# Performance work log

Hardware: AMD Instinct MI355X
Metric: run time of the kernel (lower is better)

The kernel has to match this reference:

```python
import jax, jax.numpy as jnp
import numpy as np

N, E = 100_000, 1_600_000
NFEAT, NHID, HEADS = 128, 128, 2
FOUT = NHID // 2  # per-head out feats (DGL GATConv(nfeat, nhid//2, num_heads=2))
NEG_SLOPE = 0.2
LN_EPS = 1e-5


def setup_inputs() -> dict:
    key = jax.random.key(0)
    ks = jax.random.split(key, 10)
    h = jax.random.normal(ks[0], (N, NFEAT), dtype=jnp.float32)
    src = jax.random.randint(ks[1], (E,), 0, N, dtype=jnp.int32)
    dst = jax.random.randint(ks[2], (E,), 0, N, dtype=jnp.int32)
    # GATConv params
    W = jax.random.normal(ks[3], (NFEAT, HEADS * FOUT), dtype=jnp.float32) / np.sqrt(NFEAT)
    attn_l = jax.random.normal(ks[4], (HEADS, FOUT), dtype=jnp.float32) * 0.1
    attn_r = jax.random.normal(ks[5], (HEADS, FOUT), dtype=jnp.float32) * 0.1
    bias = jnp.zeros((HEADS * FOUT,), dtype=jnp.float32)
    # LayerNorm params
    gamma = jnp.ones((NHID,), dtype=jnp.float32)
    beta = jnp.zeros((NHID,), dtype=jnp.float32)
    return {"h": h, "src": src, "dst": dst, "W": W, "attn_l": attn_l,
            "attn_r": attn_r, "bias": bias, "gamma": gamma, "beta": beta}


def reference(h, src, dst, W, attn_l, attn_r, bias, gamma, beta):
    # --- GATConv ---
    feat = (h @ W).reshape(N, HEADS, FOUT)                 # [N,H,F]
    el = jnp.einsum('nhf,hf->nh', feat, attn_l)            # [N,H]
    er = jnp.einsum('nhf,hf->nh', feat, attn_r)            # [N,H]
    e = jax.nn.leaky_relu(el[src] + er[dst], NEG_SLOPE)    # [E,H]
    # edge softmax over incoming edges of each dst node
    emax = jax.ops.segment_max(e, dst, num_segments=N)     # [N,H] (-inf for empty ok)
    expe = jnp.exp(e - emax[dst])                          # [E,H]
    denom = jax.ops.segment_sum(expe, dst, num_segments=N) # [N,H]
    alpha = expe / denom[dst]                              # [E,H]
    msg = feat[src] * alpha[:, :, None]                    # [E,H,F]
    out = jax.ops.segment_sum(msg, dst, num_segments=N)    # [N,H,F]
    x = out.reshape(N, HEADS * FOUT) + bias                # [N,NHID]
    # --- LayerNorm ---
    mu = jnp.mean(x, axis=-1, keepdims=True)
    var = jnp.mean(jnp.square(x - mu), axis=-1, keepdims=True)
    return gamma * (x - mu) * jax.lax.rsqrt(var + LN_EPS) + beta
```

## Files before the change

### kernel.cpp

```cpp
#include <hip/hip_runtime.h>
#include <hip/hip_bf16.h>

#define NFEAT 128
#define NHID  128
#define HEADS 2
#define FOUT  64
#define NEG_SLOPE 0.2f
#define LN_EPS 1e-5f
#define NPART 8
#define ECHUNK 1024
#define PACK_BLOCKS 64
#define STRIDE 64

typedef __attribute__((ext_vector_type(8))) short  short8;
typedef __attribute__((ext_vector_type(4))) float  floatx4;
typedef unsigned short ushort_t;

__device__ __forceinline__ unsigned short f32_to_bf16_bits(float x) {
    unsigned int u = __float_as_uint(x);
    unsigned int r = (u + 0x7FFF + ((u >> 16) & 1)) >> 16;
    return (unsigned short)r;
}

__global__ __launch_bounds__(256) void histscatter_pack_kernel(
    const float* __restrict__ W, ushort_t* __restrict__ pBhi,
    ushort_t* __restrict__ pBlo, const int* __restrict__ src,
    const int* __restrict__ dst, int* __restrict__ deg,
    int* __restrict__ csr_src, int E, int N)
{
    if (blockIdx.x < PACK_BLOCKS) {
        int i = blockIdx.x * 256 + threadIdx.x;
        int k = i >> 7, n = i & 127;
        float x = W[i];
        unsigned short hb = f32_to_bf16_bits(x);
        float hf = __uint_as_float(((unsigned int)hb) << 16);
        unsigned short lb = f32_to_bf16_bits(x - hf);
        int t = n >> 4, s = k >> 5, q = (k >> 3) & 3, j = k & 7;
        int lanei = (q << 4) | (n & 15);
        int idx = ((t * 4 + s) * 64 + lanei) * 8 + j;
        pBhi[idx] = hb; pBlo[idx] = lb;
        return;
    }
    int bid   = blockIdx.x - PACK_BLOCKS;
    int p     = bid & (NPART - 1);
    int chunk = bid >> 3;
    int base  = chunk * ECHUNK + threadIdx.x * 4;
    int lo = (int)(((long long)p       * N) / NPART);
    int hi = (int)(((long long)(p + 1) * N) / NPART);
    if (base + 3 < E) {
        int4 d4 = *(const int4*)(dst + base);
        int dd[4] = {d4.x, d4.y, d4.z, d4.w};
#pragma unroll
        for (int k = 0; k < 4; k++) {
            int d = dd[k];
            if (d >= lo && d < hi) {
                int pos = atomicAdd(&deg[d], 1);
                if (pos < STRIDE)
                    csr_src[(size_t)d * STRIDE + pos] = src[base + k];
            }
        }
    } else {
        for (int k = 0; k < 4; k++) {
            int i = base + k;
            if (i < E) {
                int d = dst[i];
                if (d >= lo && d < hi) {
                    int pos = atomicAdd(&deg[d], 1);
                    if (pos < STRIDE)
                        csr_src[(size_t)d * STRIDE + pos] = src[i];
                }
            }
        }
    }
}

__global__ __launch_bounds__(256) void gemm_mfma_kernel(
    const float* __restrict__ h,
    const ushort_t* __restrict__ pBhi, const ushort_t* __restrict__ pBlo,
    const float* __restrict__ attn_l, const float* __restrict__ attn_r,
    ushort_t* __restrict__ featb, float* __restrict__ el,
    float* __restrict__ er, int N)
{
    const int lane = threadIdx.x & 63;
    const int wv   = threadIdx.x >> 6;
    const int r0   = blockIdx.x * 64 + wv * 16;
    const int m    = lane & 15;
    const int q    = lane >> 4;
    int row  = r0 + m;
    int rowc = min(row, N - 1);
    const float* hrow = h + (size_t)rowc * NFEAT + q * 8;

    floatx4 acc[8];
#pragma unroll
    for (int t = 0; t < 8; t++) acc[t] = (floatx4){0.f, 0.f, 0.f, 0.f};

#pragma unroll
    for (int s = 0; s < 4; ++s) {
        float4 a0 = *(const float4*)(hrow + s * 32);
        float4 a1 = *(const float4*)(hrow + s * 32 + 4);
        float af[8] = {a0.x, a0.y, a0.z, a0.w, a1.x, a1.y, a1.z, a1.w};
        short8 ahi, alo;
#pragma unroll
        for (int jj = 0; jj < 8; jj++) {
            unsigned short hb = f32_to_bf16_bits(af[jj]);
            float hf = __uint_as_float(((unsigned int)hb) << 16);
            unsigned short lb = f32_to_bf16_bits(af[jj] - hf);
            ahi[jj] = (short)hb; alo[jj] = (short)lb;
        }
#pragma unroll
        for (int t = 0; t < 8; t++) {
            short8 bhi = *(const short8*)(pBhi + ((t * 4 + s) * 64 + lane) * 8);
            short8 blo = *(const short8*)(pBlo + ((t * 4 + s) * 64 + lane) * 8);
            acc[t] = __builtin_amdgcn_mfma_f32_16x16x32_bf16(ahi, bhi, acc[t], 0, 0, 0);
            acc[t] = __builtin_amdgcn_mfma_f32_16x16x32_bf16(ahi, blo, acc[t], 0, 0, 0);
            acc[t] = __builtin_amdgcn_mfma_f32_16x16x32_bf16(alo, bhi, acc[t], 0, 0, 0);
        }
    }
    if (r0 >= N) return;

    float alc[8], arc[8];
#pragma unroll
    for (int t = 0; t < 8; t++) {
        alc[t] = attn_l[t * 16 + m];
        arc[t] = attn_r[t * 16 + m];
    }

#pragma unroll
    for (int r = 0; r < 4; r++) {
        int rr = r0 + q * 4 + r;
        bool ok = (rr < N);
        if (ok) {
#pragma unroll
            for (int t = 0; t < 8; t++)
                featb[(size_t)rr * NHID + t * 16 + m] = f32_to_bf16_bits(acc[t][r]);
        }
        float pl0 = 0.f, pl1 = 0.f, pr0 = 0.f, pr1 = 0.f;
#pragma unroll
        for (int t = 0; t < 4; t++) {
            pl0 += acc[t][r] * alc[t];
            pr0 += acc[t][r] * arc[t];
            pl1 += acc[t + 4][r] * alc[t + 4];
            pr1 += acc[t + 4][r] * arc[t + 4];
        }
#pragma unroll
        for (int off = 1; off < 16; off <<= 1) {
            pl0 += __shfl_xor(pl0, off, 64);
            pl1 += __shfl_xor(pl1, off, 64);
            pr0 += __shfl_xor(pr0, off, 64);
            pr1 += __shfl_xor(pr1, off, 64);
        }
        if (m == 0 && ok) {
            el[rr * HEADS + 0] = pl0;
            el[rr * HEADS + 1] = pl1;
            er[rr * HEADS + 0] = pr0;
            er[rr * HEADS + 1] = pr1;
        }
    }
}

__global__ __launch_bounds__(256) void aggregate_kernel(
    const int* __restrict__ deg_arr, const int* __restrict__ csr_src,
    const ushort_t* __restrict__ featb, const float* __restrict__ el,
    const float* __restrict__ er, const float* __restrict__ bias,
    const float* __restrict__ gamma, const float* __restrict__ beta,
    float* __restrict__ out, int N)
{
    __shared__ int    s_src[4][STRIDE];
    __shared__ float2 s_e[4][STRIDE];

    const int wv   = threadIdx.x >> 6;
    const int lane = threadIdx.x & 63;
    const int node = blockIdx.x * 4 + wv;
    if (node >= N) return;

    const int deg = min(deg_arr[node], STRIDE);
    const int rs  = node * STRIDE;
    const float2 erv = *(const float2*)(er + (size_t)node * HEADS);

    float d0 = 0.f, d1 = 0.f;
    if (lane < deg) {
        int s = csr_src[rs + lane];
        float2 elv = *(const float2*)(el + (size_t)s * HEADS);
        float e0 = elv.x + erv.x; e0 = e0 > 0.f ? e0 : NEG_SLOPE * e0;
        float e1 = elv.y + erv.y; e1 = e1 > 0.f ? e1 : NEG_SLOPE * e1;
        float x0 = __expf(e0), x1 = __expf(e1);
        s_src[wv][lane] = s;
        s_e[wv][lane] = make_float2(x0, x1);
        d0 = x0; d1 = x1;
    }
#pragma unroll
    for (int off = 32; off; off >>= 1) {
        d0 += __shfl_xor(d0, off, 64);
        d1 += __shfl_xor(d1, off, 64);
    }

    const int j0   = lane * 2;
    const int hsel = lane >> 5;
    const float* s_ef = (const float*)&s_e[wv][0];
    float acc0 = 0.f, acc1 = 0.f;
    {
        int i = 0;
        for (; i + 8 <= deg; i += 8) {
            int s0 = s_src[wv][i + 0], s1 = s_src[wv][i + 1];
            int s2 = s_src[wv][i + 2], s3 = s_src[wv][i + 3];
            int s4 = s_src[wv][i + 4], s5 = s_src[wv][i + 5];
            int s6 = s_src[wv][i + 6], s7 = s_src[wv][i + 7];
            unsigned int u0 = *(const unsigned int*)(featb + (size_t)s0 * NHID + j0);
            unsigned int u1 = *(const unsigned int*)(featb + (size_t)s1 * NHID + j0);
            unsigned int u2 = *(const unsigned int*)(featb + (size_t)s2 * NHID + j0);
            unsigned int u3 = *(const unsigned int*)(featb + (size_t)s3 * NHID + j0);
            unsigned int u4 = *(const unsigned int*)(featb + (size_t)s4 * NHID + j0);
            unsigned int u5 = *(const unsigned int*)(featb + (size_t)s5 * NHID + j0);
            unsigned int u6 = *(const unsigned int*)(featb + (size_t)s6 * NHID + j0);
            unsigned int u7 = *(const unsigned int*)(featb + (size_t)s7 * NHID + j0);
            float a0 = s_ef[2 * (i + 0) + hsel];
            float a1 = s_ef[2 * (i + 1) + hsel];
            float a2 = s_ef[2 * (i + 2) + hsel];
            float a3 = s_ef[2 * (i + 3) + hsel];
            float a4 = s_ef[2 * (i + 4) + hsel];
            float a5 = s_ef[2 * (i + 5) + hsel];
            float a6 = s_ef[2 * (i + 6) + hsel];
            float a7 = s_ef[2 * (i + 7) + hsel];
            acc0 += __uint_as_float(u0 << 16) * a0;
            acc1 += __uint_as_float(u0 & 0xFFFF0000u) * a0;
            acc0 += __uint_as_float(u1 << 16) * a1;
            acc1 += __uint_as_float(u1 & 0xFFFF0000u) * a1;
            acc0 += __uint_as_float(u2 << 16) * a2;
            acc1 += __uint_as_float(u2 & 0xFFFF0000u) * a2;
            acc0 += __uint_as_float(u3 << 16) * a3;
            acc1 += __uint_as_float(u3 & 0xFFFF0000u) * a3;
            acc0 += __uint_as_float(u4 << 16) * a4;
            acc1 += __uint_as_float(u4 & 0xFFFF0000u) * a4;
            acc0 += __uint_as_float(u5 << 16) * a5;
            acc1 += __uint_as_float(u5 & 0xFFFF0000u) * a5;
            acc0 += __uint_as_float(u6 << 16) * a6;
            acc1 += __uint_as_float(u6 & 0xFFFF0000u) * a6;
            acc0 += __uint_as_float(u7 << 16) * a7;
            acc1 += __uint_as_float(u7 & 0xFFFF0000u) * a7;
        }
        for (; i + 2 <= deg; i += 2) {
            int s0 = s_src[wv][i + 0], s1 = s_src[wv][i + 1];
            unsigned int u0 = *(const unsigned int*)(featb + (size_t)s0 * NHID + j0);
            unsigned int u1 = *(const unsigned int*)(featb + (size_t)s1 * NHID + j0);
            float a0 = s_ef[2 * (i + 0) + hsel];
            float a1 = s_ef[2 * (i + 1) + hsel];
            acc0 += __uint_as_float(u0 << 16) * a0;
            acc1 += __uint_as_float(u0 & 0xFFFF0000u) * a0;
            acc0 += __uint_as_float(u1 << 16) * a1;
            acc1 += __uint_as_float(u1 & 0xFFFF0000u) * a1;
        }
        for (; i < deg; ++i) {
            int s = s_src[wv][i];
            float a = s_ef[2 * i + hsel];
            unsigned int u = *(const unsigned int*)(featb + (size_t)s * NHID + j0);
            acc0 += __uint_as_float(u << 16) * a;
            acc1 += __uint_as_float(u & 0xFFFF0000u) * a;
        }
    }
    float inv = (deg > 0) ? 1.f / ((lane < 32) ? d0 : d1) : 0.f;

    float2 bv = *(const float2*)(bias + j0);
    float x0 = acc0 * inv + bv.x;
    float x1 = acc1 * inv + bv.y;
    float s1 = x0 + x1, s2 = x0 * x0 + x1 * x1;
#pragma unroll
    for (int off = 32; off; off >>= 1) {
        s1 += __shfl_xor(s1, off, 64);
        s2 += __shfl_xor(s2, off, 64);
    }
    float mu  = s1 * (1.f / NHID);
    float var = s2 * (1.f / NHID) - mu * mu;
    float r   = rsqrtf(var + LN_EPS);
    float2 gv = *(const float2*)(gamma + j0);
    float2 tv = *(const float2*)(beta + j0);
    float2 yo = make_float2(gv.x * (x0 - mu) * r + tv.x,
                            gv.y * (x1 - mu) * r + tv.y);
    *(float2*)(out + (size_t)node * NHID + j0) = yo;
}

extern "C" void kernel_launch(void* const* d_in, const int* in_sizes, int n_in,
                              void* d_out, int out_size, void* d_ws, size_t ws_size,
                              hipStream_t stream)
{
    const float* h      = (const float*)d_in[0];
    const int*   src    = (const int*)  d_in[1];
    const int*   dst    = (const int*)  d_in[2];
    const float* W      = (const float*)d_in[3];
    const float* attn_l = (const float*)d_in[4];
    const float* attn_r = (const float*)d_in[5];
    const float* bias   = (const float*)d_in[6];
    const float* gamma  = (const float*)d_in[7];
    const float* beta   = (const float*)d_in[8];
    float* out = (float*)d_out;

    const int N = in_sizes[0] / NFEAT;
    const int E = in_sizes[1];
    const int NCHUNK = (E + ECHUNK - 1) / ECHUNK;

    ushort_t* pBhi  = (ushort_t*)d_ws;
    ushort_t* pBlo  = pBhi + NFEAT * NHID;
    ushort_t* featb = pBlo + NFEAT * NHID;
    float* el       = (float*)(featb + (size_t)N * NHID);
    float* er       = el + (size_t)N * HEADS;
    int*   deg      = (int*)(er + (size_t)N * HEADS);
    int*   csr_src  = deg + N;

    hipMemsetAsync(deg, 0, (size_t)N * 4, stream);
    histscatter_pack_kernel<<<PACK_BLOCKS + NCHUNK * NPART, 256, 0, stream>>>(
        W, pBhi, pBlo, src, dst, deg, csr_src, E, N);

    gemm_mfma_kernel<<<(N + 63) / 64, 256, 0, stream>>>(h, pBhi, pBlo, attn_l,
                                                        attn_r, featb, el, er, N);
    aggregate_kernel<<<(N + 3) / 4, 256, 0, stream>>>(deg, csr_src, featb,
                                                      el, er, bias, gamma, beta,
                                                      out, N);
}
```

Baseline: 281.5 us.

## Co-launch edge scatter with MFMA GEMM and fold degree zeroing into pack kernel

The separate memset of the degree array is replaced by extra blocks in the weight-pack kernel that zero it. The GEMM that builds features and attention logits is merged into the same launch as the atomic CSR edge scatter, with block ranges split by index. This lets the compute-heavy GEMM blocks run alongside the atomic-bound scatter blocks and removes one launch and the memset. The scatter partition index now comes from the raw block id, which still covers every partition for each chunk.

Result: slower. 289.0 us (+2.7%).

```diff
diff --git a/kernel.cpp b/kernel.cpp
--- a/kernel.cpp
+++ b/kernel.cpp
@@ -22,11 +22,9 @@
     return (unsigned short)r;
 }
 
-__global__ __launch_bounds__(256) void histscatter_pack_kernel(
+__global__ __launch_bounds__(256) void pack_init_kernel(
     const float* __restrict__ W, ushort_t* __restrict__ pBhi,
-    ushort_t* __restrict__ pBlo, const int* __restrict__ src,
-    const int* __restrict__ dst, int* __restrict__ deg,
-    int* __restrict__ csr_src, int E, int N)
+    ushort_t* __restrict__ pBlo, int* __restrict__ deg, int N)
 {
     if (blockIdx.x < PACK_BLOCKS) {
         int i = blockIdx.x * 256 + threadIdx.x;
@@ -39,10 +37,102 @@
         int lanei = (q << 4) | (n & 15);
         int idx = ((t * 4 + s) * 64 + lanei) * 8 + j;
         pBhi[idx] = hb; pBlo[idx] = lb;
+    } else {
+        int i = (blockIdx.x - PACK_BLOCKS) * 256 + threadIdx.x;
+        if (i < N) deg[i] = 0;
+    }
+}
+
+__global__ __launch_bounds__(256) void scatter_gemm_kernel(
+    const int* __restrict__ src, const int* __restrict__ dst,
+    int* __restrict__ deg, int* __restrict__ csr_src,
+    const float* __restrict__ h,
+    const ushort_t* __restrict__ pBhi, const ushort_t* __restrict__ pBlo,
+    const float* __restrict__ attn_l, const float* __restrict__ attn_r,
+    ushort_t* __restrict__ featb, float* __restrict__ el,
+    float* __restrict__ er, int E, int N, int NGB)
+{
+    if ((int)blockIdx.x < NGB) {
+        const int lane = threadIdx.x & 63;
+        const int wv   = threadIdx.x >> 6;
+        const int r0   = blockIdx.x * 64 + wv * 16;
+        const int m    = lane & 15;
+        const int q    = lane >> 4;
+        int row  = r0 + m;
+        int rowc = min(row, N - 1);
+        const float* hrow = h + (size_t)rowc * NFEAT + q * 8;
+
+        floatx4 acc[8];
+#pragma unroll
+        for (int t = 0; t < 8; t++) acc[t] = (floatx4){0.f, 0.f, 0.f, 0.f};
+
+#pragma unroll
+        for (int s = 0; s < 4; ++s) {
+            float4 a0 = *(const float4*)(hrow + s * 32);
+            float4 a1 = *(const float4*)(hrow + s * 32 + 4);
+            float af[8] = {a0.x, a0.y, a0.z, a0.w, a1.x, a1.y, a1.z, a1.w};
+            short8 ahi, alo;
+#pragma unroll
+            for (int jj = 0; jj < 8; jj++) {
+                unsigned short hb = f32_to_bf16_bits(af[jj]);
+                float hf = __uint_as_float(((unsigned int)hb) << 16);
+                unsigned short lb = f32_to_bf16_bits(af[jj] - hf);
+                ahi[jj] = (short)hb; alo[jj] = (short)lb;
+            }
+#pragma unroll
+            for (int t = 0; t < 8; t++) {
+                short8 bhi = *(const short8*)(pBhi + ((t * 4 + s) * 64 + lane) * 8);
+                short8 blo = *(const short8*)(pBlo + ((t * 4 + s) * 64 + lane) * 8);
+                acc[t] = __builtin_amdgcn_mfma_f32_16x16x32_bf16(ahi, bhi, acc[t], 0, 0, 0);
+                acc[t] = __builtin_amdgcn_mfma_f32_16x16x32_bf16(ahi, blo, acc[t], 0, 0, 0);
+                acc[t] = __builtin_amdgcn_mfma_f32_16x16x32_bf16(alo, bhi, acc[t], 0, 0, 0);
+            }
+        }
+        if (r0 >= N) return;
+
+        float alc[8], arc[8];
+#pragma unroll
+        for (int t = 0; t < 8; t++) {
+            alc[t] = attn_l[t * 16 + m];
+            arc[t] = attn_r[t * 16 + m];
+        }
+
+#pragma unroll
+        for (int r = 0; r < 4; r++) {
+            int rr = r0 + q * 4 + r;
+            bool ok = (rr < N);
+            if (ok) {
+#pragma unroll
+                for (int t = 0; t < 8; t++)
+                    featb[(size_t)rr * NHID + t * 16 + m] = f32_to_bf16_bits(acc[t][r]);
+            }
+            float pl0 = 0.f, pl1 = 0.f, pr0 = 0.f, pr1 = 0.f;
+#pragma unroll
+            for (int t = 0; t < 4; t++) {
+                pl0 += acc[t][r] * alc[t];
+                pr0 += acc[t][r] * arc[t];
+                pl1 += acc[t + 4][r] * alc[t + 4];
+                pr1 += acc[t + 4][r] * arc[t + 4];
+            }
+#pragma unroll
+            for (int off = 1; off < 16; off <<= 1) {
+                pl0 += __shfl_xor(pl0, off, 64);
+                pl1 += __shfl_xor(pl1, off, 64);
+                pr0 += __shfl_xor(pr0, off, 64);
+                pr1 += __shfl_xor(pr1, off, 64);
+            }
+            if (m == 0 && ok) {
+                el[rr * HEADS + 0] = pl0;
+                el[rr * HEADS + 1] = pl1;
+                er[rr * HEADS + 0] = pr0;
+                er[rr * HEADS + 1] = pr1;
+            }
+        }
         return;
     }
-    int bid   = blockIdx.x - PACK_BLOCKS;
-    int p     = bid & (NPART - 1);
+
+    int bid   = (int)blockIdx.x - NGB;
+    int p     = (int)blockIdx.x & (NPART - 1);
     int chunk = bid >> 3;
     int base  = chunk * ECHUNK + threadIdx.x * 4;
     int lo = (int)(((long long)p       * N) / NPART);
@@ -70,90 +160,6 @@
                         csr_src[(size_t)d * STRIDE + pos] = src[i];
                 }
             }
-        }
-    }
-}
-
-__global__ __launch_bounds__(256) void gemm_mfma_kernel(
-    const float* __restrict__ h,
-    const ushort_t* __restrict__ pBhi, const ushort_t* __restrict__ pBlo,
-    const float* __restrict__ attn_l, const float* __restrict__ attn_r,
-    ushort_t* __restrict__ featb, float* __restrict__ el,
-    float* __restrict__ er, int N)
-{
-    const int lane = threadIdx.x & 63;
-    const int wv   = threadIdx.x >> 6;
-    const int r0   = blockIdx.x * 64 + wv * 16;
-    const int m    = lane & 15;
-    const int q    = lane >> 4;
-    int row  = r0 + m;
-    int rowc = min(row, N - 1);
-    const float* hrow = h + (size_t)rowc * NFEAT + q * 8;
-
-    floatx4 acc[8];
-#pragma unroll
-    for (int t = 0; t < 8; t++) acc[t] = (floatx4){0.f, 0.f, 0.f, 0.f};
-
-#pragma unroll
-    for (int s = 0; s < 4; ++s) {
-        float4 a0 = *(const float4*)(hrow + s * 32);
-        float4 a1 = *(const float4*)(hrow + s * 32 + 4);
-        float af[8] = {a0.x, a0.y, a0.z, a0.w, a1.x, a1.y, a1.z, a1.w};
-        short8 ahi, alo;
-#pragma unroll
-        for (int jj = 0; jj < 8; jj++) {
-            unsigned short hb = f32_to_bf16_bits(af[jj]);
-            float hf = __uint_as_float(((unsigned int)hb) << 16);
-            unsigned short lb = f32_to_bf16_bits(af[jj] - hf);
-            ahi[jj] = (short)hb; alo[jj] = (short)lb;
-        }
-#pragma unroll
-        for (int t = 0; t < 8; t++) {
-            short8 bhi = *(const short8*)(pBhi + ((t * 4 + s) * 64 + lane) * 8);
-            short8 blo = *(const short8*)(pBlo + ((t * 4 + s) * 64 + lane) * 8);
-            acc[t] = __builtin_amdgcn_mfma_f32_16x16x32_bf16(ahi, bhi, acc[t], 0, 0, 0);
-            acc[t] = __builtin_amdgcn_mfma_f32_16x16x32_bf16(ahi, blo, acc[t], 0, 0, 0);
-            acc[t] = __builtin_amdgcn_mfma_f32_16x16x32_bf16(alo, bhi, acc[t], 0, 0, 0);
-        }
-    }
-    if (r0 >= N) return;
-
-    float alc[8], arc[8];
-#pragma unroll
-    for (int t = 0; t < 8; t++) {
-        alc[t] = attn_l[t * 16 + m];
-        arc[t] = attn_r[t * 16 + m];
-    }
-
-#pragma unroll
-    for (int r = 0; r < 4; r++) {
-        int rr = r0 + q * 4 + r;
-        bool ok = (rr < N);
-        if (ok) {
-#pragma unroll
-            for (int t = 0; t < 8; t++)
-                featb[(size_t)rr * NHID + t * 16 + m] = f32_to_bf16_bits(acc[t][r]);
-        }
-        float pl0 = 0.f, pl1 = 0.f, pr0 = 0.f, pr1 = 0.f;
-#pragma unroll
-        for (int t = 0; t < 4; t++) {
-            pl0 += acc[t][r] * alc[t];
-            pr0 += acc[t][r] * arc[t];
-            pl1 += acc[t + 4][r] * alc[t + 4];
-            pr1 += acc[t + 4][r] * arc[t + 4];
-        }
-#pragma unroll
-        for (int off = 1; off < 16; off <<= 1) {
-            pl0 += __shfl_xor(pl0, off, 64);
-            pl1 += __shfl_xor(pl1, off, 64);
-            pr0 += __shfl_xor(pr0, off, 64);
-            pr1 += __shfl_xor(pr1, off, 64);
-        }
-        if (m == 0 && ok) {
-            el[rr * HEADS + 0] = pl0;
-            el[rr * HEADS + 1] = pl1;
-            er[rr * HEADS + 0] = pr0;
-            er[rr * HEADS + 1] = pr1;
         }
     }
 }
@@ -296,6 +302,8 @@
     const int N = in_sizes[0] / NFEAT;
     const int E = in_sizes[1];
     const int NCHUNK = (E + ECHUNK - 1) / ECHUNK;
+    const int NGB    = (N + 63) / 64;
+    const int NZB    = (N + 255) / 256;
 
     ushort_t* pBhi  = (ushort_t*)d_ws;
     ushort_t* pBlo  = pBhi + NFEAT * NHID;
@@ -305,12 +313,13 @@
     int*   deg      = (int*)(er + (size_t)N * HEADS);
     int*   csr_src  = deg + N;
 
-    hipMemsetAsync(deg, 0, (size_t)N * 4, stream);
-    histscatter_pack_kernel<<<PACK_BLOCKS + NCHUNK * NPART, 256, 0, stream>>>(
-        W, pBhi, pBlo, src, dst, deg, csr_src, E, N);
-
-    gemm_mfma_kernel<<<(N + 63) / 64, 256, 0, stream>>>(h, pBhi, pBlo, attn_l,
-                                                        attn_r, featb, el, er, N);
+    pack_init_kernel<<<PACK_BLOCKS + NZB, 256, 0, stream>>>(
+        W, pBhi, pBlo, deg, N);
+
+    scatter_gemm_kernel<<<NGB + NCHUNK * NPART, 256, 0, stream>>>(
+        src, dst, deg, csr_src, h, pBhi, pBlo, attn_l, attn_r,
+        featb, el, er, E, N, NGB);
+
     aggregate_kernel<<<(N + 3) / 4, 256, 0, stream>>>(deg, csr_src, featb,
                                                       el, er, bias, gamma, beta,
                                                       out, N);
```
